# Optimization experiments

Measured on AMD Instinct MI355X. Metric: run time of the kernel, lower is better.

Reference implementation:

```python
import jax, jax.numpy as jnp
import numpy as np

N = 50000      # nodes
E = 400000     # edges (before self-loops)
F_IN = 256     # input_dim
HID = 64       # hidden_dim (per-head)
H = 4          # heads
OUT = 16       # output_dim
NEG_SLOPE = 0.2


def _gat_layer(x, W, a_src, a_dst, b, src, dst):
    # x: [N, Fin], W: [Fin, H*HID], a_src/a_dst: [H, HID], b: [H*HID]
    n = x.shape[0]
    h = (x @ W).reshape(n, H, HID)                        # [N,H,D]
    es = jnp.einsum('nhd,hd->nh', h, a_src)               # [N,H]
    ed = jnp.einsum('nhd,hd->nh', h, a_dst)               # [N,H]
    e = jax.nn.leaky_relu(es[src] + ed[dst], NEG_SLOPE)   # [E,H]
    m = jax.ops.segment_max(e, dst, num_segments=n)       # [N,H] segment softmax (stable)
    m = jnp.where(jnp.isfinite(m), m, 0.0)
    p = jnp.exp(e - m[dst])
    s = jax.ops.segment_sum(p, dst, num_segments=n)
    alpha = p / (s[dst] + 1e-16)                          # [E,H]
    out = jax.ops.segment_sum(h[src] * alpha[:, :, None], dst, num_segments=n)  # [N,H,D]
    return out.reshape(n, H * HID) + b


def setup_inputs() -> dict:
    key = jax.random.key(0)
    ks = jax.random.split(key, 24)
    lin = lambda k, i, o: (jax.random.normal(k, (i, o), jnp.float32) / np.sqrt(i)).astype(jnp.float32)
    att = lambda k: (jax.random.normal(k, (H, HID), jnp.float32) * 0.1).astype(jnp.float32)
    FH = H * HID  # 256
    inp = {
        'x': jax.random.normal(ks[0], (N, F_IN), jnp.float32),
        'edge_index': jax.random.randint(ks[1], (2, E), 0, N, dtype=jnp.int64),
        'W1': lin(ks[2], F_IN, FH), 'a1_src': att(ks[3]), 'a1_dst': att(ks[4]), 'b1': jnp.zeros((FH,), jnp.float32),
        'W2': lin(ks[5], FH, FH),   'a2_src': att(ks[6]), 'a2_dst': att(ks[7]), 'b2': jnp.zeros((FH,), jnp.float32),
        'W3': lin(ks[8], FH, FH),   'a3_src': att(ks[9]), 'a3_dst': att(ks[10]), 'b3': jnp.zeros((FH,), jnp.float32),
        'pW1': lin(ks[11], FH, HID), 'pb1': jnp.zeros((HID,), jnp.float32),
        'pW2': lin(ks[12], HID, HID), 'pb2': jnp.zeros((HID,), jnp.float32),
        'cW1': lin(ks[13], FH, HID), 'cb1': jnp.zeros((HID,), jnp.float32),
        'cW2': lin(ks[14], HID, OUT), 'cb2': jnp.zeros((OUT,), jnp.float32),
    }
    return inp


def reference(x, edge_index, W1, a1_src, a1_dst, b1, W2, a2_src, a2_dst, b2,
              W3, a3_src, a3_dst, b3, pW1, pb1, pW2, pb2, cW1, cb1, cW2, cb2):
    n = x.shape[0]
    loop = jnp.arange(n, dtype=edge_index.dtype)          # PyG GATConv adds self-loops
    src = jnp.concatenate([edge_index[0], loop])
    dst = jnp.concatenate([edge_index[1], loop])
    h = jax.nn.elu(_gat_layer(x, W1, a1_src, a1_dst, b1, src, dst))
    h = jax.nn.elu(_gat_layer(h, W2, a2_src, a2_dst, b2, src, dst))
    h = _gat_layer(h, W3, a3_src, a3_dst, b3, src, dst)   # [N, 256]
    logits = jax.nn.relu(h @ cW1 + cb1) @ cW2 + cb2       # classifier (dropout inactive, eval)
    proj = jax.nn.relu(h @ pW1 + pb1) @ pW2 + pb2         # projection head
    return jax.nn.log_softmax(logits, axis=1), proj
```

## Files before the change

kernel.cpp:

```cpp
#include <hip/hip_runtime.h>
#include <hip/hip_bf16.h>

#define NN 50000
#define EE 400000
#define TE (EE + NN)
#define SCAN_B ((NN + 255) / 256)

typedef float f4 __attribute__((ext_vector_type(4)));
typedef __bf16 b8 __attribute__((ext_vector_type(8)));
typedef unsigned short us8 __attribute__((ext_vector_type(8)));

__device__ __forceinline__ float b2f(unsigned short u) {
    union { unsigned int i; float f; } c; c.i = ((unsigned int)u) << 16; return c.f;
}
__device__ __forceinline__ unsigned short f2b(float x) {
    union { unsigned int i; float f; } c; c.f = x;
    unsigned int i = c.i;
    return (unsigned short)((i + 0x7FFFu + ((i >> 16) & 1u)) >> 16);
}
__device__ __forceinline__ int clampi(int v, int lo, int hi) {
    return v < lo ? lo : (v > hi ? hi : v);
}

#define PO_WT    0
#define PO_ATT   196608
#define PO_BT    198912
#define PO_BIAS  231680
#define PO_PW2   231808
#define PO_PB2   235904
#define PO_CW2   235968
#define PO_CB2   236992
#define PO_BT2   237008
#define PO_BIAS2 253392
#define PO_TOTAL 253520

__global__ void detect_kernel(const int* __restrict__ ei, const unsigned int* __restrict__ xw,
                              int* __restrict__ flag) {
    int lane = threadIdx.x;
    int bad = (lane < 16 && ei[2 * lane + 1] != 0) ? 1 : 0;
    int cnt = 0;
#pragma unroll
    for (int k = 0; k < 4; k++) {
        int i = lane + k * 64;
        unsigned short lo = (unsigned short)(xw[i] & 0xFFFFu);
        int e = (lo >> 7) & 0xFF;
        if (e >= 120 && e <= 132) cnt++;
    }
    unsigned long long anybad = __ballot(bad != 0);
#pragma unroll
    for (int off = 1; off < 64; off <<= 1) cnt += __shfl_xor(cnt, off, 64);
    if (lane == 0) {
        flag[0] = (anybad == 0ULL) ? 1 : 0;
        flag[1] = (cnt >= 128) ? 1 : 0;
    }
}

__global__ __launch_bounds__(256) void convx_kernel(const void* __restrict__ src,
                                                    unsigned short* __restrict__ dst,
                                                    const int* __restrict__ flag) {
    int i = blockIdx.x * 256 + threadIdx.x;
    if (i >= NN * 256 / 4) return;
    if (flag[1]) {
        ((ushort4*)dst)[i] = ((const ushort4*)src)[i];
    } else {
        float4 v = ((const float4*)src)[i];
        ushort4 o; o.x = f2b(v.x); o.y = f2b(v.y); o.z = f2b(v.z); o.w = f2b(v.w);
        ((ushort4*)dst)[i] = o;
    }
}

__device__ __forceinline__ float ldf(const void* p, int i, int bf) {
    return bf ? b2f(((const unsigned short*)p)[i]) : ((const float*)p)[i];
}
__global__ __launch_bounds__(256) void prep_kernel(
    const void* W1, const void* W2, const void* W3,
    const void* as1, const void* ad1, const void* b1,
    const void* as2, const void* ad2, const void* b2,
    const void* as3, const void* ad3, const void* b3,
    const void* pW1, const void* pb1, const void* pW2, const void* pb2,
    const void* cW1, const void* cb1, const void* cW2, const void* cb2,
    unsigned short* __restrict__ P, const int* __restrict__ flag) {
    int idx = blockIdx.x * 256 + threadIdx.x;
    if (idx >= PO_TOTAL) return;
    int bf = flag[1];
    float v;
    if (idx < PO_ATT) {
        int l = idx / 65536, r = idx % 65536;
        int n = r >> 8, k = r & 255;
        const void* W = (l == 0) ? W1 : (l == 1) ? W2 : W3;
        v = ldf(W, k * 256 + n, bf);
    } else if (idx < PO_BT) {
        int r = idx - PO_ATT;
        int l = r / 768, w = r % 768, which = w >> 8, j = w & 255;
        const void* s;
        if (which == 0) s = (l == 0) ? as1 : (l == 1) ? as2 : as3;
        else if (which == 1) s = (l == 0) ? ad1 : (l == 1) ? ad2 : ad3;
        else s = (l == 0) ? b1 : (l == 1) ? b2 : b3;
        v = ldf(s, j, bf);
    } else if (idx < PO_BIAS) {
        int r3 = idx - PO_BT;
        int r = r3 >> 8, k = r3 & 255;
        v = (r < 64) ? ldf(cW1, k * 64 + r, bf) : ldf(pW1, k * 64 + (r - 64), bf);
    } else if (idx < PO_PW2) {
        int r = idx - PO_BIAS;
        v = (r < 64) ? ldf(cb1, r, bf) : ldf(pb1, r - 64, bf);
    } else if (idx < PO_PB2) {
        v = ldf(pW2, idx - PO_PW2, bf);
    } else if (idx < PO_CW2) {
        v = ldf(pb2, idx - PO_PB2, bf);
    } else if (idx < PO_CB2) {
        v = ldf(cW2, idx - PO_CW2, bf);
    } else if (idx < PO_BT2) {
        v = ldf(cb2, idx - PO_CB2, bf);
    } else if (idx < PO_BIAS2) {
        int r2 = idx - PO_BT2;
        int r = r2 >> 7, k = r2 & 127;
        if (r < 16) v = (k < 64) ? ldf(cW2, k * 16 + r, bf) : 0.f;
        else if (r < 80) v = (k >= 64) ? ldf(pW2, (k - 64) * 64 + (r - 16), bf) : 0.f;
        else v = 0.f;
    } else {
        int r = idx - PO_BIAS2;
        v = (r < 16) ? ldf(cb2, r, bf) : (r < 80 ? ldf(pb2, r - 16, bf) : 0.f);
    }
    P[idx] = f2b(v);
}

__device__ __forceinline__ void edge_decode(const int* __restrict__ ei, int mode64, int e,
                                            int& src, int& dst) {
    if (e < EE) {
        if (mode64) { src = ei[2 * e]; dst = ei[2 * EE + 2 * e]; }
        else        { src = ei[e];     dst = ei[EE + e]; }
        src = clampi(src, 0, NN - 1);
        dst = clampi(dst, 0, NN - 1);
    } else {
        src = dst = e - EE;
    }
}

__global__ __launch_bounds__(256) void zero_kernel(int* __restrict__ deg, int* __restrict__ cursor) {
    int i = blockIdx.x * 256 + threadIdx.x;
    if (i < NN) { deg[i] = 0; cursor[i] = 0; }
}

__global__ void deg_kernel(const int* __restrict__ ei, const int* __restrict__ flag,
                           int* __restrict__ deg) {
    int e = blockIdx.x * 256 + threadIdx.x;
    if (e >= TE) return;
    int src, dst;
    edge_decode(ei, flag[0], e, src, dst);
    atomicAdd(&deg[dst], 1);
}

__global__ __launch_bounds__(256) void scanA_kernel(const int* __restrict__ deg,
                                                    int* __restrict__ offs, int* __restrict__ bsum) {
    __shared__ int s[256];
    int t = threadIdx.x, i = blockIdx.x * 256 + t;
    int v = (i < NN) ? deg[i] : 0;
    s[t] = v;
    __syncthreads();
    for (int off = 1; off < 256; off <<= 1) {
        int x = (t >= off) ? s[t - off] : 0;
        __syncthreads();
        s[t] += x;
        __syncthreads();
    }
    if (i < NN) offs[i] = s[t] - v;
    if (t == 255) bsum[blockIdx.x] = s[255];
}
__global__ __launch_bounds__(256) void scanB_kernel(int* __restrict__ bsum) {
    __shared__ int s[256];
    int t = threadIdx.x;
    int v = (t < SCAN_B) ? bsum[t] : 0;
    s[t] = v;
    __syncthreads();
    for (int off = 1; off < 256; off <<= 1) {
        int x = (t >= off) ? s[t - off] : 0;
        __syncthreads();
        s[t] += x;
        __syncthreads();
    }
    if (t < SCAN_B) bsum[t] = s[t] - v;
}
__global__ __launch_bounds__(256) void scanC_kernel(int* __restrict__ offs,
                                                    const int* __restrict__ bsum) {
    int t = threadIdx.x, i = blockIdx.x * 256 + t;
    if (i < NN) offs[i] += bsum[blockIdx.x];
    if (i == 0) offs[NN] = TE;
}

__global__ void scatter_kernel(const int* __restrict__ ei, const int* __restrict__ flag,
                               const int* __restrict__ offs,
                               int* __restrict__ cursor, int* __restrict__ srcs,
                               int* __restrict__ dsts) {
    int e = blockIdx.x * 256 + threadIdx.x;
    if (e >= TE) return;
    int src, dst;
    edge_decode(ei, flag[0], e, src, dst);
    int pos = atomicAdd(&cursor[dst], 1);
    int slot = offs[dst] + pos;
    if (slot >= 0 && slot < TE) { srcs[slot] = src; dsts[slot] = dst; }
}

__device__ __forceinline__ void async_ld16(const unsigned short* g, unsigned short* l) {
    __builtin_amdgcn_global_load_lds(
        (const __attribute__((address_space(1))) unsigned int*)g,
        (__attribute__((address_space(3))) unsigned int*)l, 16, 0, 0);
}

__global__ __launch_bounds__(256) void gemm_bt_kernel(
    const unsigned short* __restrict__ A, const unsigned short* __restrict__ Bt,
    unsigned short* __restrict__ C, int M, int Nc, int K,
    const unsigned short* __restrict__ bias, int relu, int outf32, int final,
    const unsigned short* __restrict__ asrc, const unsigned short* __restrict__ adst,
    float* __restrict__ es, float* __restrict__ ed) {
    __shared__ unsigned short As[2][128 * 32];
    __shared__ unsigned short Bs[2][128 * 32];
    int tid = threadIdx.x;
    int lane = tid & 63;
    int wave = tid >> 6;
    int wr = wave >> 1, wc = wave & 1;
    int m0 = blockIdx.x * 128;
    int n0 = blockIdx.y * 128;
    f4 acc[4][4];
#pragma unroll
    for (int i = 0; i < 4; i++)
#pragma unroll
        for (int j = 0; j < 4; j++) acc[i][j] = (f4){0.f, 0.f, 0.f, 0.f};

    int rin = lane >> 2;
    int qsl = lane & 3;
    int qg  = qsl ^ ((rin >> 1) & 3);
    int rsel = lane & 15;
    int q16 = lane >> 4;
    int slotq = q16 ^ ((rsel >> 1) & 3);

    auto stage = [&](int b, int kt) {
#pragma unroll
        for (int t = 0; t < 4; t++) {
            int seg = wave * 4 + t;
            if (seg < 8) {
                int r = seg * 16 + rin;
                int gm = m0 + r;
                if (gm < M)
                    async_ld16(A + (size_t)gm * K + kt + qg * 8, &As[b][seg * 512]);
            } else {
                int r = (seg - 8) * 16 + rin;
                int gn = n0 + r;
                async_ld16(Bt + (size_t)gn * K + kt + qg * 8, &Bs[b][(seg - 8) * 512]);
            }
        }
    };

    int nk = K >> 5;
    stage(0, 0);
    __syncthreads();
    for (int s = 0; s < nk; s++) {
        int cur = s & 1;
        if (s + 1 < nk) stage(cur ^ 1, (s + 1) << 5);
        b8 af[4], bfv[4];
#pragma unroll
        for (int i = 0; i < 4; i++) {
            af[i]  = *(const b8*)(&As[cur][(wr * 64 + i * 16 + rsel) * 32 + slotq * 8]);
            bfv[i] = *(const b8*)(&Bs[cur][(wc * 64 + i * 16 + rsel) * 32 + slotq * 8]);
        }
#pragma unroll
        for (int i = 0; i < 4; i++)
#pragma unroll
            for (int j = 0; j < 4; j++)
                acc[i][j] = __builtin_amdgcn_mfma_f32_16x16x32_bf16(af[i], bfv[j], acc[i][j], 0, 0, 0);
        __syncthreads();
    }
    int cl = lane & 15, rq = lane >> 4;
    if (es) {
        int head = blockIdx.y * 2 + wc;
        float asv[4], adv[4];
#pragma unroll
        for (int j = 0; j < 4; j++) {
            asv[j] = b2f(asrc[head * 64 + j * 16 + cl]);
            adv[j] = b2f(adst[head * 64 + j * 16 + cl]);
        }
#pragma unroll
        for (int i = 0; i < 4; i++) {
            float pes[4], ped[4];
#pragma unroll
            for (int r = 0; r < 4; r++) {
                float se = 0.f, de = 0.f;
#pragma unroll
                for (int j = 0; j < 4; j++) {
                    se += acc[i][j][r] * asv[j];
                    de += acc[i][j][r] * adv[j];
                }
                pes[r] = se; ped[r] = de;
            }
#pragma unroll
            for (int off = 1; off < 16; off <<= 1) {
#pragma unroll
                for (int r = 0; r < 4; r++) {
                    pes[r] += __shfl_xor(pes[r], off, 64);
                    ped[r] += __shfl_xor(ped[r], off, 64);
                }
            }
            if (cl == 0) {
#pragma unroll
                for (int r = 0; r < 4; r++) {
                    int row = m0 + wr * 64 + i * 16 + rq * 4 + r;
                    if (row < M) {
                        es[(size_t)row * 4 + head] = pes[r];
                        ed[(size_t)row * 4 + head] = ped[r];
                    }
                }
            }
        }
    }
    if (final) {
        float* flog  = (float*)C;
        float* fproj = flog + (size_t)M * 16;
#pragma unroll
        for (int i = 0; i < 4; i++) {
#pragma unroll
            for (int r = 0; r < 4; r++) {
                int row = m0 + wr * 64 + i * 16 + rq * 4 + r;
                if (row >= M) continue;
                if (wc == 0) {
                    float lv = acc[i][0][r] + b2f(bias[cl]);
                    float mx = lv;
#pragma unroll
                    for (int off = 1; off < 16; off <<= 1) mx = fmaxf(mx, __shfl_xor(mx, off, 64));
                    float se = __expf(lv - mx);
#pragma unroll
                    for (int off = 1; off < 16; off <<= 1) se += __shfl_xor(se, off, 64);
                    flog[(size_t)row * 16 + cl] = lv - mx - __logf(se);
#pragma unroll
                    for (int j = 1; j < 4; j++) {
                        float pv = acc[i][j][r] + b2f(bias[j * 16 + cl]);
                        fproj[(size_t)row * 64 + j * 16 + cl - 16] = pv;
                    }
                } else {
                    float pv = acc[i][0][r] + b2f(bias[64 + cl]);
                    fproj[(size_t)row * 64 + 48 + cl] = pv;
                }
            }
        }
        return;
    }
#pragma unroll
    for (int j = 0; j < 4; j++) {
        int col = n0 + wc * 64 + j * 16 + cl;
        float bv = bias ? b2f(bias[col]) : 0.0f;
#pragma unroll
        for (int i = 0; i < 4; i++) {
#pragma unroll
            for (int r = 0; r < 4; r++) {
                int row = m0 + wr * 64 + i * 16 + rq * 4 + r;
                if (row < M) {
                    float v = acc[i][j][r] + bv;
                    if (relu) v = fmaxf(v, 0.0f);
                    if (outf32) ((float*)C)[(size_t)row * Nc + col] = v;
                    else C[(size_t)row * Nc + col] = f2b(v);
                }
            }
        }
    }
}

__global__ __launch_bounds__(256) void wexp_kernel(
    const float* __restrict__ es, const float* __restrict__ ed,
    const int* __restrict__ srcs, const int* __restrict__ dsts,
    float* __restrict__ wbuf) {
    int j = blockIdx.x * 256 + threadIdx.x;
    if (j >= TE) return;
    int s = srcs[j], d = dsts[j];
    float4 a = ((const float4*)es)[s];
    float4 b = ((const float4*)ed)[d];
    float v0 = a.x + b.x, v1 = a.y + b.y, v2 = a.z + b.z, v3 = a.w + b.w;
    v0 = v0 > 0.f ? v0 : 0.2f * v0; v1 = v1 > 0.f ? v1 : 0.2f * v1;
    v2 = v2 > 0.f ? v2 : 0.2f * v2; v3 = v3 > 0.f ? v3 : 0.2f * v3;
    ((float4*)wbuf)[j] = make_float4(__expf(v0), __expf(v1), __expf(v2), __expf(v3));
}

__global__ __launch_bounds__(256) void aggr_kernel(
    const unsigned short* __restrict__ H, const float* __restrict__ wbuf,
    const int* __restrict__ offs, const int* __restrict__ srcs,
    const unsigned short* __restrict__ bias, unsigned short* __restrict__ out, int N, int elu) {
    int gw = (blockIdx.x * 256 + threadIdx.x) >> 6;
    int lane = threadIdx.x & 63;
    if (gw >= N) return;
    int half = lane >> 5;
    int lh = lane & 31;
    int ch = lh << 3;
    int head = lh >> 3;
    int j0 = offs[gw];
    int j1 = offs[gw + 1];
    int d = j1 - j0;
    float a0 = 0.f, a1 = 0.f, a2 = 0.f, a3 = 0.f;
    float a4 = 0.f, a5 = 0.f, a6 = 0.f, a7 = 0.f;
    float sw = 0.f;
    int nfull8 = d & ~7;
    for (int t = 0; t < nfull8; t += 8) {
        int base = j0 + t + half * 4;
        int s0 = srcs[base], s1 = srcs[base + 1], s2 = srcs[base + 2], s3 = srcs[base + 3];
        float w0 = wbuf[(size_t)base * 4 + head];
        float w1 = wbuf[(size_t)(base + 1) * 4 + head];
        float w2 = wbuf[(size_t)(base + 2) * 4 + head];
        float w3 = wbuf[(size_t)(base + 3) * 4 + head];
        us8 h0 = *(const us8*)(H + (size_t)s0 * 256 + ch);
        us8 h1 = *(const us8*)(H + (size_t)s1 * 256 + ch);
        us8 h2 = *(const us8*)(H + (size_t)s2 * 256 + ch);
        us8 h3 = *(const us8*)(H + (size_t)s3 * 256 + ch);
        sw += (w0 + w1) + (w2 + w3);
        a0 += w0 * b2f(h0[0]) + w1 * b2f(h1[0]) + w2 * b2f(h2[0]) + w3 * b2f(h3[0]);
        a1 += w0 * b2f(h0[1]) + w1 * b2f(h1[1]) + w2 * b2f(h2[1]) + w3 * b2f(h3[1]);
        a2 += w0 * b2f(h0[2]) + w1 * b2f(h1[2]) + w2 * b2f(h2[2]) + w3 * b2f(h3[2]);
        a3 += w0 * b2f(h0[3]) + w1 * b2f(h1[3]) + w2 * b2f(h2[3]) + w3 * b2f(h3[3]);
        a4 += w0 * b2f(h0[4]) + w1 * b2f(h1[4]) + w2 * b2f(h2[4]) + w3 * b2f(h3[4]);
        a5 += w0 * b2f(h0[5]) + w1 * b2f(h1[5]) + w2 * b2f(h2[5]) + w3 * b2f(h3[5]);
        a6 += w0 * b2f(h0[6]) + w1 * b2f(h1[6]) + w2 * b2f(h2[6]) + w3 * b2f(h3[6]);
        a7 += w0 * b2f(h0[7]) + w1 * b2f(h1[7]) + w2 * b2f(h2[7]) + w3 * b2f(h3[7]);
    }
    int jt = j0 + nfull8;
    if (j1 - jt >= 4) {
        int base = jt + half * 2;
        int s0 = srcs[base], s1 = srcs[base + 1];
        float w0 = wbuf[(size_t)base * 4 + head];
        float w1 = wbuf[(size_t)(base + 1) * 4 + head];
        us8 h0 = *(const us8*)(H + (size_t)s0 * 256 + ch);
        us8 h1 = *(const us8*)(H + (size_t)s1 * 256 + ch);
        sw += w0 + w1;
        a0 += w0 * b2f(h0[0]) + w1 * b2f(h1[0]);
        a1 += w0 * b2f(h0[1]) + w1 * b2f(h1[1]);
        a2 += w0 * b2f(h0[2]) + w1 * b2f(h1[2]);
        a3 += w0 * b2f(h0[3]) + w1 * b2f(h1[3]);
        a4 += w0 * b2f(h0[4]) + w1 * b2f(h1[4]);
        a5 += w0 * b2f(h0[5]) + w1 * b2f(h1[5]);
        a6 += w0 * b2f(h0[6]) + w1 * b2f(h1[6]);
        a7 += w0 * b2f(h0[7]) + w1 * b2f(h1[7]);
        jt += 4;
    }
    for (int j = jt + half; j < j1; j += 2) {
        int sA = srcs[j];
        float wA = wbuf[(size_t)j * 4 + head];
        us8 hA = *(const us8*)(H + (size_t)sA * 256 + ch);
        sw += wA;
        a0 += wA * b2f(hA[0]); a1 += wA * b2f(hA[1]);
        a2 += wA * b2f(hA[2]); a3 += wA * b2f(hA[3]);
        a4 += wA * b2f(hA[4]); a5 += wA * b2f(hA[5]);
        a6 += wA * b2f(hA[6]); a7 += wA * b2f(hA[7]);
    }
    sw += __shfl_xor(sw, 32, 64);
    a0 += __shfl_xor(a0, 32, 64); a1 += __shfl_xor(a1, 32, 64);
    a2 += __shfl_xor(a2, 32, 64); a3 += __shfl_xor(a3, 32, 64);
    a4 += __shfl_xor(a4, 32, 64); a5 += __shfl_xor(a5, 32, 64);
    a6 += __shfl_xor(a6, 32, 64); a7 += __shfl_xor(a7, 32, 64);
    if (half == 0) {
        float rs = 1.f / (sw + 1e-16f);
        us8 bv = *(const us8*)(bias + ch);
        float r0 = a0 * rs + b2f(bv[0]), r1 = a1 * rs + b2f(bv[1]);
        float r2 = a2 * rs + b2f(bv[2]), r3 = a3 * rs + b2f(bv[3]);
        float r4 = a4 * rs + b2f(bv[4]), r5 = a5 * rs + b2f(bv[5]);
        float r6 = a6 * rs + b2f(bv[6]), r7 = a7 * rs + b2f(bv[7]);
        if (elu) {
            r0 = r0 > 0.f ? r0 : __expf(r0) - 1.f;
            r1 = r1 > 0.f ? r1 : __expf(r1) - 1.f;
            r2 = r2 > 0.f ? r2 : __expf(r2) - 1.f;
            r3 = r3 > 0.f ? r3 : __expf(r3) - 1.f;
            r4 = r4 > 0.f ? r4 : __expf(r4) - 1.f;
            r5 = r5 > 0.f ? r5 : __expf(r5) - 1.f;
            r6 = r6 > 0.f ? r6 : __expf(r6) - 1.f;
            r7 = r7 > 0.f ? r7 : __expf(r7) - 1.f;
        }
        us8 o;
        o[0] = f2b(r0); o[1] = f2b(r1); o[2] = f2b(r2); o[3] = f2b(r3);
        o[4] = f2b(r4); o[5] = f2b(r5); o[6] = f2b(r6); o[7] = f2b(r7);
        *(us8*)(out + (size_t)gw * 256 + ch) = o;
    }
}

extern "C" void kernel_launch(void* const* d_in, const int* in_sizes, int n_in,
                              void* d_out, int out_size, void* d_ws, size_t ws_size,
                              hipStream_t stream) {
    (void)in_sizes; (void)n_in; (void)out_size; (void)ws_size;
    const int* ei = (const int*)d_in[1];

    char* p = (char*)d_ws;
    auto take = [&](size_t bytes) -> void* {
        void* r = (void*)p;
        p += (bytes + 255) & ~(size_t)255;
        return r;
    };
    int* flag   = (int*)take(256);
    int* deg    = (int*)take((size_t)NN * 4);
    int* cursor = (int*)take((size_t)NN * 4);
    int* offs   = (int*)take((size_t)(NN + 1) * 4);
    int* bsum   = (int*)take(256 * 4);
    int* srcs   = (int*)take((size_t)TE * 4);
    int* dsts   = (int*)take((size_t)TE * 4);
    float* es   = (float*)take((size_t)NN * 16);
    float* ed   = (float*)take((size_t)NN * 16);
    float* wbuf = (float*)take((size_t)TE * 16);
    unsigned short* bufH = (unsigned short*)take((size_t)NN * 256 * 2);
    unsigned short* buf1 = (unsigned short*)take((size_t)NN * 256 * 2);
    unsigned short* buf2 = (unsigned short*)take((size_t)NN * 256 * 2);
    unsigned short* P    = (unsigned short*)take((size_t)PO_TOTAL * 2);
    unsigned short* xb = buf2;
    unsigned short* tbuf = bufH;

    detect_kernel<<<1, 64, 0, stream>>>(ei, (const unsigned int*)d_in[0], flag);
    convx_kernel<<<NN * 256 / 4 / 256, 256, 0, stream>>>(d_in[0], xb, flag);
    prep_kernel<<<(PO_TOTAL + 255) / 256, 256, 0, stream>>>(
        d_in[2], d_in[6], d_in[10],
        d_in[3], d_in[4], d_in[5],
        d_in[7], d_in[8], d_in[9],
        d_in[11], d_in[12], d_in[13],
        d_in[14], d_in[15], d_in[16], d_in[17],
        d_in[18], d_in[19], d_in[20], d_in[21],
        P, flag);

    zero_kernel<<<SCAN_B, 256, 0, stream>>>(deg, cursor);
    deg_kernel<<<(TE + 255) / 256, 256, 0, stream>>>(ei, flag, deg);
    scanA_kernel<<<SCAN_B, 256, 0, stream>>>(deg, offs, bsum);
    scanB_kernel<<<1, 256, 0, stream>>>(bsum);
    scanC_kernel<<<SCAN_B, 256, 0, stream>>>(offs, bsum);
    scatter_kernel<<<(TE + 255) / 256, 256, 0, stream>>>(ei, flag, offs, cursor, srcs, dsts);

    const unsigned short* X = xb;
    unsigned short* outbuf[3] = {buf1, buf2, buf1};
    for (int l = 0; l < 3; l++) {
        const unsigned short* Wt  = P + PO_WT + l * 65536;
        const unsigned short* asr = P + PO_ATT + l * 768;
        const unsigned short* adr = P + PO_ATT + l * 768 + 256;
        const unsigned short* bcb = P + PO_ATT + l * 768 + 512;
        gemm_bt_kernel<<<dim3((NN + 127) / 128, 2), 256, 0, stream>>>(
            X, Wt, bufH, NN, 256, 256, nullptr, 0, 0, 0, asr, adr, es, ed);
        wexp_kernel<<<(TE + 255) / 256, 256, 0, stream>>>(es, ed, srcs, dsts, wbuf);
        aggr_kernel<<<12500, 256, 0, stream>>>(bufH, wbuf, offs, srcs, bcb, outbuf[l], NN, (l < 2) ? 1 : 0);
        X = outbuf[l];
    }
    gemm_bt_kernel<<<dim3((NN + 127) / 128, 1), 256, 0, stream>>>(
        X, P + PO_BT, tbuf, NN, 128, 256, P + PO_BIAS, 1, 0, 0, nullptr, nullptr, nullptr, nullptr);
    gemm_bt_kernel<<<dim3((NN + 127) / 128, 1), 256, 0, stream>>>(
        tbuf, P + PO_BT2, (unsigned short*)d_out, NN, 128, 128, P + PO_BIAS2, 0, 0, 1, nullptr, nullptr, nullptr, nullptr);
}
```

Before: 441.4 us.

## Fuse edge-weight exp into aggregation, merge head GEMMs and setup kernels

Removes the wexp kernel and its per-edge weight buffer: aggregation now recomputes leaky-relu and exp from per-node es/ed, which saves writing and reading a large per-edge buffer each layer. The two classifier/projection GEMMs are fused into one kernel that keeps the hidden tile in LDS. The detect, zero and scanB/C kernels are folded into neighbouring kernels, and the dsts array is dropped. This cuts launches and memory traffic at the cost of redundant detection work in every block and extra exp per edge per lane.

```diff
diff --git a/kernel.cpp b/kernel.cpp
--- a/kernel.cpp
+++ b/kernel.cpp
@@ -34,33 +34,44 @@
 #define PO_BIAS2 253392
 #define PO_TOTAL 253520
 
-__global__ void detect_kernel(const int* __restrict__ ei, const unsigned int* __restrict__ xw,
-                              int* __restrict__ flag) {
-    int lane = threadIdx.x;
-    int bad = (lane < 16 && ei[2 * lane + 1] != 0) ? 1 : 0;
-    int cnt = 0;
-#pragma unroll
-    for (int k = 0; k < 4; k++) {
-        int i = lane + k * 64;
-        unsigned short lo = (unsigned short)(xw[i] & 0xFFFFu);
-        int e = (lo >> 7) & 0xFF;
-        if (e >= 120 && e <= 132) cnt++;
-    }
-    unsigned long long anybad = __ballot(bad != 0);
-#pragma unroll
-    for (int off = 1; off < 64; off <<= 1) cnt += __shfl_xor(cnt, off, 64);
-    if (lane == 0) {
-        flag[0] = (anybad == 0ULL) ? 1 : 0;
-        flag[1] = (cnt >= 128) ? 1 : 0;
-    }
+__device__ __forceinline__ int detect_xbf(const unsigned int* xw, int tid, int* sm) {
+    if (tid < 64) {
+        int cnt = 0;
+#pragma unroll
+        for (int k = 0; k < 4; k++) {
+            int i = tid + k * 64;
+            unsigned short lo = (unsigned short)(xw[i] & 0xFFFFu);
+            int e = (lo >> 7) & 0xFF;
+            if (e >= 120 && e <= 132) cnt++;
+        }
+#pragma unroll
+        for (int off = 1; off < 64; off <<= 1) cnt += __shfl_xor(cnt, off, 64);
+        if (tid == 0) *sm = (cnt >= 128) ? 1 : 0;
+    }
+    __syncthreads();
+    return *sm;
+}
+__device__ __forceinline__ int detect_e64(const int* ei, int tid, int* sm) {
+    if (tid < 64) {
+        int bad = (tid < 16 && ei[2 * tid + 1] != 0) ? 1 : 0;
+        unsigned long long anybad = __ballot(bad != 0);
+        if (tid == 0) *sm = (anybad == 0ULL) ? 1 : 0;
+    }
+    __syncthreads();
+    return *sm;
 }
 
 __global__ __launch_bounds__(256) void convx_kernel(const void* __restrict__ src,
                                                     unsigned short* __restrict__ dst,
-                                                    const int* __restrict__ flag) {
-    int i = blockIdx.x * 256 + threadIdx.x;
+                                                    int* __restrict__ deg,
+                                                    int* __restrict__ cursor) {
+    __shared__ int sm;
+    int tid = threadIdx.x;
+    int bf = detect_xbf((const unsigned int*)src, tid, &sm);
+    int i = blockIdx.x * 256 + tid;
+    if (blockIdx.x < SCAN_B && i < NN) { deg[i] = 0; cursor[i] = 0; }
     if (i >= NN * 256 / 4) return;
-    if (flag[1]) {
+    if (bf) {
         ((ushort4*)dst)[i] = ((const ushort4*)src)[i];
     } else {
         float4 v = ((const float4*)src)[i];
@@ -73,16 +84,19 @@
     return bf ? b2f(((const unsigned short*)p)[i]) : ((const float*)p)[i];
 }
 __global__ __launch_bounds__(256) void prep_kernel(
+    const void* __restrict__ xsrc,
     const void* W1, const void* W2, const void* W3,
     const void* as1, const void* ad1, const void* b1,
     const void* as2, const void* ad2, const void* b2,
     const void* as3, const void* ad3, const void* b3,
     const void* pW1, const void* pb1, const void* pW2, const void* pb2,
     const void* cW1, const void* cb1, const void* cW2, const void* cb2,
-    unsigned short* __restrict__ P, const int* __restrict__ flag) {
-    int idx = blockIdx.x * 256 + threadIdx.x;
+    unsigned short* __restrict__ P) {
+    __shared__ int sm;
+    int tid = threadIdx.x;
+    int bf = detect_xbf((const unsigned int*)xsrc, tid, &sm);
+    int idx = blockIdx.x * 256 + tid;
     if (idx >= PO_TOTAL) return;
-    int bf = flag[1];
     float v;
     if (idx < PO_ATT) {
         int l = idx / 65536, r = idx % 65536;
@@ -137,17 +151,15 @@
     }
 }
 
-__global__ __launch_bounds__(256) void zero_kernel(int* __restrict__ deg, int* __restrict__ cursor) {
-    int i = blockIdx.x * 256 + threadIdx.x;
-    if (i < NN) { deg[i] = 0; cursor[i] = 0; }
-}
-
-__global__ void deg_kernel(const int* __restrict__ ei, const int* __restrict__ flag,
-                           int* __restrict__ deg) {
-    int e = blockIdx.x * 256 + threadIdx.x;
+__global__ __launch_bounds__(256) void deg_kernel(const int* __restrict__ ei,
+                                                  int* __restrict__ deg) {
+    __shared__ int sm;
+    int tid = threadIdx.x;
+    int mode64 = detect_e64(ei, tid, &sm);
+    int e = blockIdx.x * 256 + tid;
     if (e >= TE) return;
     int src, dst;
-    edge_decode(ei, flag[0], e, src, dst);
+    edge_decode(ei, mode64, e, src, dst);
     atomicAdd(&deg[dst], 1);
 }
 
@@ -167,7 +179,8 @@
     if (i < NN) offs[i] = s[t] - v;
     if (t == 255) bsum[blockIdx.x] = s[255];
 }
-__global__ __launch_bounds__(256) void scanB_kernel(int* __restrict__ bsum) {
+__global__ __launch_bounds__(256) void scanBC_kernel(int* __restrict__ offs,
+                                                     const int* __restrict__ bsum) {
     __shared__ int s[256];
     int t = threadIdx.x;
     int v = (t < SCAN_B) ? bsum[t] : 0;
@@ -179,26 +192,26 @@
         s[t] += x;
         __syncthreads();
     }
-    if (t < SCAN_B) bsum[t] = s[t] - v;
-}
-__global__ __launch_bounds__(256) void scanC_kernel(int* __restrict__ offs,
-                                                    const int* __restrict__ bsum) {
-    int t = threadIdx.x, i = blockIdx.x * 256 + t;
-    if (i < NN) offs[i] += bsum[blockIdx.x];
+    int add = (blockIdx.x > 0) ? s[blockIdx.x - 1] : 0;
+    int i = blockIdx.x * 256 + t;
+    if (i < NN) offs[i] += add;
     if (i == 0) offs[NN] = TE;
 }
 
-__global__ void scatter_kernel(const int* __restrict__ ei, const int* __restrict__ flag,
-                               const int* __restrict__ offs,
-                               int* __restrict__ cursor, int* __restrict__ srcs,
-                               int* __restrict__ dsts) {
-    int e = blockIdx.x * 256 + threadIdx.x;
+__global__ __launch_bounds__(256) void scatter_kernel(const int* __restrict__ ei,
+                                                      const int* __restrict__ offs,
+                                                      int* __restrict__ cursor,
+                                                      int* __restrict__ srcs) {
+    __shared__ int sm;
+    int tid = threadIdx.x;
+    int mode64 = detect_e64(ei, tid, &sm);
+    int e = blockIdx.x * 256 + tid;
     if (e >= TE) return;
     int src, dst;
-    edge_decode(ei, flag[0], e, src, dst);
+    edge_decode(ei, mode64, e, src, dst);
     int pos = atomicAdd(&cursor[dst], 1);
     int slot = offs[dst] + pos;
-    if (slot >= 0 && slot < TE) { srcs[slot] = src; dsts[slot] = dst; }
+    if (slot >= 0 && slot < TE) srcs[slot] = src;
 }
 
 __device__ __forceinline__ void async_ld16(const unsigned short* g, unsigned short* l) {
@@ -209,10 +222,10 @@
 
 __global__ __launch_bounds__(256) void gemm_bt_kernel(
     const unsigned short* __restrict__ A, const unsigned short* __restrict__ Bt,
-    unsigned short* __restrict__ C, int M, int Nc, int K,
-    const unsigned short* __restrict__ bias, int relu, int outf32, int final,
+    unsigned short* __restrict__ C, int M,
     const unsigned short* __restrict__ asrc, const unsigned short* __restrict__ adst,
     float* __restrict__ es, float* __restrict__ ed) {
+    const int K = 256, Nc = 256;
     __shared__ unsigned short As[2][128 * 32];
     __shared__ unsigned short Bs[2][128 * 32];
     int tid = threadIdx.x;
@@ -251,7 +264,7 @@
         }
     };
 
-    int nk = K >> 5;
+    const int nk = K >> 5;
     stage(0, 0);
     __syncthreads();
     for (int s = 0; s < nk; s++) {
@@ -271,7 +284,7 @@
         __syncthreads();
     }
     int cl = lane & 15, rq = lane >> 4;
-    if (es) {
+    {
         int head = blockIdx.y * 2 + wc;
         float asv[4], adv[4];
 #pragma unroll
@@ -312,74 +325,167 @@
             }
         }
     }
-    if (final) {
-        float* flog  = (float*)C;
-        float* fproj = flog + (size_t)M * 16;
+#pragma unroll
+    for (int j = 0; j < 4; j++) {
+        int col = n0 + wc * 64 + j * 16 + cl;
 #pragma unroll
         for (int i = 0; i < 4; i++) {
 #pragma unroll
             for (int r = 0; r < 4; r++) {
                 int row = m0 + wr * 64 + i * 16 + rq * 4 + r;
-                if (row >= M) continue;
-                if (wc == 0) {
-                    float lv = acc[i][0][r] + b2f(bias[cl]);
-                    float mx = lv;
-#pragma unroll
-                    for (int off = 1; off < 16; off <<= 1) mx = fmaxf(mx, __shfl_xor(mx, off, 64));
-                    float se = __expf(lv - mx);
-#pragma unroll
-                    for (int off = 1; off < 16; off <<= 1) se += __shfl_xor(se, off, 64);
-                    flog[(size_t)row * 16 + cl] = lv - mx - __logf(se);
-#pragma unroll
-                    for (int j = 1; j < 4; j++) {
-                        float pv = acc[i][j][r] + b2f(bias[j * 16 + cl]);
-                        fproj[(size_t)row * 64 + j * 16 + cl - 16] = pv;
-                    }
-                } else {
-                    float pv = acc[i][0][r] + b2f(bias[64 + cl]);
-                    fproj[(size_t)row * 64 + 48 + cl] = pv;
+                if (row < M) C[(size_t)row * Nc + col] = f2b(acc[i][j][r]);
+            }
+        }
+    }
+}
+
+__global__ __launch_bounds__(256) void gemm_final_kernel(
+    const unsigned short* __restrict__ A, const unsigned short* __restrict__ Bt1,
+    const unsigned short* __restrict__ bias1, const unsigned short* __restrict__ B2g,
+    const unsigned short* __restrict__ bias2,
+    float* __restrict__ flog, float* __restrict__ fproj, int M) {
+    const int K = 256;
+    __shared__ unsigned short smem[32768];
+    unsigned short* As0 = smem;
+    unsigned short* Bs0 = smem + 8192;
+    unsigned short* T   = smem;
+    unsigned short* B2s = smem + 16384;
+    int tid = threadIdx.x;
+    int lane = tid & 63;
+    int wave = tid >> 6;
+    int wr = wave >> 1, wc = wave & 1;
+    int m0 = blockIdx.x * 128;
+    f4 acc[4][4];
+#pragma unroll
+    for (int i = 0; i < 4; i++)
+#pragma unroll
+        for (int j = 0; j < 4; j++) acc[i][j] = (f4){0.f, 0.f, 0.f, 0.f};
+
+    int rin = lane >> 2;
+    int qsl = lane & 3;
+    int qg  = qsl ^ ((rin >> 1) & 3);
+    int rsel = lane & 15;
+    int q16 = lane >> 4;
+    int slotq = q16 ^ ((rsel >> 1) & 3);
+
+#pragma unroll
+    for (int t = 0; t < 8; t++) {
+        int row = t * 16 + wave * 4 + (lane >> 4);
+        int chunk = lane & 15;
+        async_ld16(B2g + row * 128 + ((chunk ^ (row & 15)) << 3),
+                   B2s + (t * 16 + wave * 4) * 128);
+    }
+
+    auto stage = [&](int b, int kt) {
+#pragma unroll
+        for (int t = 0; t < 4; t++) {
+            int seg = wave * 4 + t;
+            if (seg < 8) {
+                int r = seg * 16 + rin;
+                int gm = m0 + r;
+                if (gm < M)
+                    async_ld16(A + (size_t)gm * K + kt + qg * 8, &As0[b * 4096 + seg * 512]);
+            } else {
+                int r = (seg - 8) * 16 + rin;
+                async_ld16(Bt1 + (size_t)r * K + kt + qg * 8, &Bs0[b * 4096 + (seg - 8) * 512]);
+            }
+        }
+    };
+
+    stage(0, 0);
+    __syncthreads();
+    for (int s = 0; s < 8; s++) {
+        int cur = s & 1;
+        if (s + 1 < 8) stage(cur ^ 1, (s + 1) << 5);
+        b8 af[4], bfv[4];
+#pragma unroll
+        for (int i = 0; i < 4; i++) {
+            af[i]  = *(const b8*)(&As0[cur * 4096 + (wr * 64 + i * 16 + rsel) * 32 + slotq * 8]);
+            bfv[i] = *(const b8*)(&Bs0[cur * 4096 + (wc * 64 + i * 16 + rsel) * 32 + slotq * 8]);
+        }
+#pragma unroll
+        for (int i = 0; i < 4; i++)
+#pragma unroll
+            for (int j = 0; j < 4; j++)
+                acc[i][j] = __builtin_amdgcn_mfma_f32_16x16x32_bf16(af[i], bfv[j], acc[i][j], 0, 0, 0);
+        __syncthreads();
+    }
+
+    int cl = lane & 15, rq = lane >> 4;
+#pragma unroll
+    for (int j = 0; j < 4; j++) {
+        int col = wc * 64 + j * 16 + cl;
+        float bv = b2f(bias1[col]);
+        int chunk = col >> 3, cr = col & 7;
+#pragma unroll
+        for (int i = 0; i < 4; i++) {
+#pragma unroll
+            for (int r = 0; r < 4; r++) {
+                int row = wr * 64 + i * 16 + rq * 4 + r;
+                float v = fmaxf(acc[i][j][r] + bv, 0.0f);
+                T[row * 128 + ((chunk ^ (row & 15)) << 3) + cr] = f2b(v);
+            }
+        }
+    }
+    __syncthreads();
+
+    f4 acc2[4][4];
+#pragma unroll
+    for (int i = 0; i < 4; i++)
+#pragma unroll
+        for (int j = 0; j < 4; j++) acc2[i][j] = (f4){0.f, 0.f, 0.f, 0.f};
+#pragma unroll
+    for (int s2 = 0; s2 < 4; s2++) {
+        int kc = s2 * 4 + q16;
+        b8 af2[4], bf2[4];
+#pragma unroll
+        for (int i = 0; i < 4; i++) {
+            int row = wr * 64 + i * 16 + rsel;
+            af2[i] = *(const b8*)(&T[row * 128 + ((kc ^ (row & 15)) << 3)]);
+        }
+#pragma unroll
+        for (int j = 0; j < 4; j++) {
+            int col = wc * 64 + j * 16 + rsel;
+            bf2[j] = *(const b8*)(&B2s[col * 128 + ((kc ^ (col & 15)) << 3)]);
+        }
+#pragma unroll
+        for (int i = 0; i < 4; i++)
+#pragma unroll
+            for (int j = 0; j < 4; j++)
+                acc2[i][j] = __builtin_amdgcn_mfma_f32_16x16x32_bf16(af2[i], bf2[j], acc2[i][j], 0, 0, 0);
+    }
+
+#pragma unroll
+    for (int i = 0; i < 4; i++) {
+#pragma unroll
+        for (int r = 0; r < 4; r++) {
+            int row = m0 + wr * 64 + i * 16 + rq * 4 + r;
+            if (row >= M) continue;
+            if (wc == 0) {
+                float lv = acc2[i][0][r] + b2f(bias2[cl]);
+                float mx = lv;
+#pragma unroll
+                for (int off = 1; off < 16; off <<= 1) mx = fmaxf(mx, __shfl_xor(mx, off, 64));
+                float se = __expf(lv - mx);
+#pragma unroll
+                for (int off = 1; off < 16; off <<= 1) se += __shfl_xor(se, off, 64);
+                flog[(size_t)row * 16 + cl] = lv - mx - __logf(se);
+#pragma unroll
+                for (int j = 1; j < 4; j++) {
+                    float pv = acc2[i][j][r] + b2f(bias2[j * 16 + cl]);
+                    fproj[(size_t)row * 64 + j * 16 + cl - 16] = pv;
                 }
-            }
-        }
-        return;
-    }
-#pragma unroll
-    for (int j = 0; j < 4; j++) {
-        int col = n0 + wc * 64 + j * 16 + cl;
-        float bv = bias ? b2f(bias[col]) : 0.0f;
-#pragma unroll
-        for (int i = 0; i < 4; i++) {
-#pragma unroll
-            for (int r = 0; r < 4; r++) {
-                int row = m0 + wr * 64 + i * 16 + rq * 4 + r;
-                if (row < M) {
-                    float v = acc[i][j][r] + bv;
-                    if (relu) v = fmaxf(v, 0.0f);
-                    if (outf32) ((float*)C)[(size_t)row * Nc + col] = v;
-                    else C[(size_t)row * Nc + col] = f2b(v);
-                }
-            }
-        }
-    }
-}
-
-__global__ __launch_bounds__(256) void wexp_kernel(
-    const float* __restrict__ es, const float* __restrict__ ed,
-    const int* __restrict__ srcs, const int* __restrict__ dsts,
-    float* __restrict__ wbuf) {
-    int j = blockIdx.x * 256 + threadIdx.x;
-    if (j >= TE) return;
-    int s = srcs[j], d = dsts[j];
-    float4 a = ((const float4*)es)[s];
-    float4 b = ((const float4*)ed)[d];
-    float v0 = a.x + b.x, v1 = a.y + b.y, v2 = a.z + b.z, v3 = a.w + b.w;
-    v0 = v0 > 0.f ? v0 : 0.2f * v0; v1 = v1 > 0.f ? v1 : 0.2f * v1;
-    v2 = v2 > 0.f ? v2 : 0.2f * v2; v3 = v3 > 0.f ? v3 : 0.2f * v3;
-    ((float4*)wbuf)[j] = make_float4(__expf(v0), __expf(v1), __expf(v2), __expf(v3));
+            } else {
+                float pv = acc2[i][0][r] + b2f(bias2[64 + cl]);
+                fproj[(size_t)row * 64 + 48 + cl] = pv;
+            }
+        }
+    }
 }
 
 __global__ __launch_bounds__(256) void aggr_kernel(
-    const unsigned short* __restrict__ H, const float* __restrict__ wbuf,
+    const unsigned short* __restrict__ H, const float* __restrict__ es,
+    const float* __restrict__ ed,
     const int* __restrict__ offs, const int* __restrict__ srcs,
     const unsigned short* __restrict__ bias, unsigned short* __restrict__ out, int N, int elu) {
     int gw = (blockIdx.x * 256 + threadIdx.x) >> 6;
@@ -389,24 +495,29 @@
     int lh = lane & 31;
     int ch = lh << 3;
     int head = lh >> 3;
-    int j0 = offs[gw];
-    int j1 = offs[gw + 1];
+    int j0 = clampi(offs[gw], 0, TE);
+    int j1 = clampi(offs[gw + 1], j0, TE);
     int d = j1 - j0;
+    float edh = ed[gw * 4 + head];
     float a0 = 0.f, a1 = 0.f, a2 = 0.f, a3 = 0.f;
     float a4 = 0.f, a5 = 0.f, a6 = 0.f, a7 = 0.f;
     float sw = 0.f;
     int nfull8 = d & ~7;
     for (int t = 0; t < nfull8; t += 8) {
         int base = j0 + t + half * 4;
-        int s0 = srcs[base], s1 = srcs[base + 1], s2 = srcs[base + 2], s3 = srcs[base + 3];
-        float w0 = wbuf[(size_t)base * 4 + head];
-        float w1 = wbuf[(size_t)(base + 1) * 4 + head];
-        float w2 = wbuf[(size_t)(base + 2) * 4 + head];
-        float w3 = wbuf[(size_t)(base + 3) * 4 + head];
+        int s0 = clampi(srcs[base], 0, NN - 1), s1 = clampi(srcs[base + 1], 0, NN - 1);
+        int s2 = clampi(srcs[base + 2], 0, NN - 1), s3 = clampi(srcs[base + 3], 0, NN - 1);
+        float e0 = es[s0 * 4 + head], e1 = es[s1 * 4 + head];
+        float e2 = es[s2 * 4 + head], e3 = es[s3 * 4 + head];
         us8 h0 = *(const us8*)(H + (size_t)s0 * 256 + ch);
         us8 h1 = *(const us8*)(H + (size_t)s1 * 256 + ch);
         us8 h2 = *(const us8*)(H + (size_t)s2 * 256 + ch);
         us8 h3 = *(const us8*)(H + (size_t)s3 * 256 + ch);
+        float v0 = e0 + edh; v0 = v0 > 0.f ? v0 : 0.2f * v0;
+        float v1 = e1 + edh; v1 = v1 > 0.f ? v1 : 0.2f * v1;
+        float v2 = e2 + edh; v2 = v2 > 0.f ? v2 : 0.2f * v2;
+        float v3 = e3 + edh; v3 = v3 > 0.f ? v3 : 0.2f * v3;
+        float w0 = __expf(v0), w1 = __expf(v1), w2 = __expf(v2), w3 = __expf(v3);
         sw += (w0 + w1) + (w2 + w3);
         a0 += w0 * b2f(h0[0]) + w1 * b2f(h1[0]) + w2 * b2f(h2[0]) + w3 * b2f(h3[0]);
         a1 += w0 * b2f(h0[1]) + w1 * b2f(h1[1]) + w2 * b2f(h2[1]) + w3 * b2f(h3[1]);
@@ -420,11 +531,13 @@
     int jt = j0 + nfull8;
     if (j1 - jt >= 4) {
         int base = jt + half * 2;
-        int s0 = srcs[base], s1 = srcs[base + 1];
-        float w0 = wbuf[(size_t)base * 4 + head];
-        float w1 = wbuf[(size_t)(base + 1) * 4 + head];
+        int s0 = clampi(srcs[base], 0, NN - 1), s1 = clampi(srcs[base + 1], 0, NN - 1);
+        float e0 = es[s0 * 4 + head], e1 = es[s1 * 4 + head];
         us8 h0 = *(const us8*)(H + (size_t)s0 * 256 + ch);
         us8 h1 = *(const us8*)(H + (size_t)s1 * 256 + ch);
+        float v0 = e0 + edh; v0 = v0 > 0.f ? v0 : 0.2f * v0;
+        float v1 = e1 + edh; v1 = v1 > 0.f ? v1 : 0.2f * v1;
+        float w0 = __expf(v0), w1 = __expf(v1);
         sw += w0 + w1;
         a0 += w0 * b2f(h0[0]) + w1 * b2f(h1[0]);
         a1 += w0 * b2f(h0[1]) + w1 * b2f(h1[1]);
@@ -437,9 +550,11 @@
         jt += 4;
     }
     for (int j = jt + half; j < j1; j += 2) {
-        int sA = srcs[j];
-        float wA = wbuf[(size_t)j * 4 + head];
+        int sA = clampi(srcs[j], 0, NN - 1);
+        float eA = es[sA * 4 + head];
         us8 hA = *(const us8*)(H + (size_t)sA * 256 + ch);
+        float vA = eA + edh; vA = vA > 0.f ? vA : 0.2f * vA;
+        float wA = __expf(vA);
         sw += wA;
         a0 += wA * b2f(hA[0]); a1 += wA * b2f(hA[1]);
         a2 += wA * b2f(hA[2]); a3 += wA * b2f(hA[3]);
@@ -487,40 +602,34 @@
         p += (bytes + 255) & ~(size_t)255;
         return r;
     };
-    int* flag   = (int*)take(256);
     int* deg    = (int*)take((size_t)NN * 4);
     int* cursor = (int*)take((size_t)NN * 4);
     int* offs   = (int*)take((size_t)(NN + 1) * 4);
     int* bsum   = (int*)take(256 * 4);
     int* srcs   = (int*)take((size_t)TE * 4);
-    int* dsts   = (int*)take((size_t)TE * 4);
     float* es   = (float*)take((size_t)NN * 16);
     float* ed   = (float*)take((size_t)NN * 16);
-    float* wbuf = (float*)take((size_t)TE * 16);
     unsigned short* bufH = (unsigned short*)take((size_t)NN * 256 * 2);
     unsigned short* buf1 = (unsigned short*)take((size_t)NN * 256 * 2);
     unsigned short* buf2 = (unsigned short*)take((size_t)NN * 256 * 2);
     unsigned short* P    = (unsigned short*)take((size_t)PO_TOTAL * 2);
     unsigned short* xb = buf2;
-    unsigned short* tbuf = bufH;
-
-    detect_kernel<<<1, 64, 0, stream>>>(ei, (const unsigned int*)d_in[0], flag);
-    convx_kernel<<<NN * 256 / 4 / 256, 256, 0, stream>>>(d_in[0], xb, flag);
+
+    convx_kernel<<<NN * 256 / 4 / 256, 256, 0, stream>>>(d_in[0], xb, deg, cursor);
     prep_kernel<<<(PO_TOTAL + 255) / 256, 256, 0, stream>>>(
+        d_in[0],
         d_in[2], d_in[6], d_in[10],
         d_in[3], d_in[4], d_in[5],
         d_in[7], d_in[8], d_in[9],
         d_in[11], d_in[12], d_in[13],
         d_in[14], d_in[15], d_in[16], d_in[17],
         d_in[18], d_in[19], d_in[20], d_in[21],
-        P, flag);
-
-    zero_kernel<<<SCAN_B, 256, 0, stream>>>(deg, cursor);
-    deg_kernel<<<(TE + 255) / 256, 256, 0, stream>>>(ei, flag, deg);
+        P);
+
+    deg_kernel<<<(TE + 255) / 256, 256, 0, stream>>>(ei, deg);
     scanA_kernel<<<SCAN_B, 256, 0, stream>>>(deg, offs, bsum);
-    scanB_kernel<<<1, 256, 0, stream>>>(bsum);
-    scanC_kernel<<<SCAN_B, 256, 0, stream>>>(offs, bsum);
-    scatter_kernel<<<(TE + 255) / 256, 256, 0, stream>>>(ei, flag, offs, cursor, srcs, dsts);
+    scanBC_kernel<<<SCAN_B, 256, 0, stream>>>(offs, bsum);
+    scatter_kernel<<<(TE + 255) / 256, 256, 0, stream>>>(ei, offs, cursor, srcs);
 
     const unsigned short* X = xb;
     unsigned short* outbuf[3] = {buf1, buf2, buf1};
@@ -530,13 +639,12 @@
         const unsigned short* adr = P + PO_ATT + l * 768 + 256;
         const unsigned short* bcb = P + PO_ATT + l * 768 + 512;
         gemm_bt_kernel<<<dim3((NN + 127) / 128, 2), 256, 0, stream>>>(
-            X, Wt, bufH, NN, 256, 256, nullptr, 0, 0, 0, asr, adr, es, ed);
-        wexp_kernel<<<(TE + 255) / 256, 256, 0, stream>>>(es, ed, srcs, dsts, wbuf);
-        aggr_kernel<<<12500, 256, 0, stream>>>(bufH, wbuf, offs, srcs, bcb, outbuf[l], NN, (l < 2) ? 1 : 0);
+            X, Wt, bufH, NN, asr, adr, es, ed);
+        aggr_kernel<<<12500, 256, 0, stream>>>(bufH, es, ed, offs, srcs, bcb, outbuf[l], NN, (l < 2) ? 1 : 0);
         X = outbuf[l];
     }
-    gemm_bt_kernel<<<dim3((NN + 127) / 128, 1), 256, 0, stream>>>(
-        X, P + PO_BT, tbuf, NN, 128, 256, P + PO_BIAS, 1, 0, 0, nullptr, nullptr, nullptr, nullptr);
-    gemm_bt_kernel<<<dim3((NN + 127) / 128, 1), 256, 0, stream>>>(
-        tbuf, P + PO_BT2, (unsigned short*)d_out, NN, 128, 128, P + PO_BIAS2, 0, 0, 1, nullptr, nullptr, nullptr, nullptr);
-}
+    float* out0 = (float*)d_out;
+    float* out1 = out0 + (size_t)NN * 16;
+    gemm_final_kernel<<<(NN + 127) / 128, 256, 0, stream>>>(
+        X, P + PO_BT, P + PO_BIAS, P + PO_BT2, P + PO_BIAS2, out0, out1, NN);
+}
```

Measured after the change: 409.1 us. 7.3% less time.
